# Optimization experiments

Measured on AMD Instinct MI355X. Metric: run time of the kernel, lower is better.

Reference implementation:

```python
import jax, jax.numpy as jnp
import numpy as np

N_NODES = 50000
N_EDGES = 800000
IN_CH = 256
OUT_CH = 128
HID = 2 * OUT_CH  # 256
N_GRAPHS = 64


def setup_inputs() -> dict:
    key = jax.random.key(0)
    k = jax.random.split(key, 8)
    x = jax.random.normal(k[0], (N_NODES, IN_CH), dtype=jnp.float32)
    edge_index = jax.random.randint(k[1], (2, N_EDGES), 0, N_NODES, dtype=jnp.int64)
    batch = jnp.sort(jax.random.randint(k[2], (N_NODES,), 0, N_GRAPHS, dtype=jnp.int64))
    # GCNConv parameters (glorot-ish init)
    W1 = jax.random.normal(k[3], (IN_CH, HID), dtype=jnp.float32) / np.sqrt(IN_CH)
    b1 = jnp.zeros((HID,), dtype=jnp.float32)
    W2 = jax.random.normal(k[4], (HID, OUT_CH), dtype=jnp.float32) / np.sqrt(HID)
    b2 = jnp.zeros((OUT_CH,), dtype=jnp.float32)
    return {"x": x, "W1": W1, "b1": b1, "W2": W2, "b2": b2,
            "edge_index": edge_index, "batch": batch}


def _gcn_conv(x, W, b, src, dst, n):
    """PyG GCNConv: transform, then sym-normalized aggregation with self-loops."""
    h = x @ W  # [N, F_out]
    # degree over destination nodes, including the added self-loop
    deg = jnp.zeros((n,), dtype=h.dtype).at[dst].add(1.0) + 1.0
    dinv = jax.lax.rsqrt(deg)
    norm = dinv[src] * dinv[dst]            # [E]
    agg = jnp.zeros_like(h).at[dst].add(h[src] * norm[:, None])
    agg = agg + h * (1.0 / deg)[:, None]    # self-loop contribution: deg_i^{-1}
    return agg + b


def reference(x, W1, b1, W2, b2, edge_index, batch):
    src, dst = edge_index[0], edge_index[1]
    # dropout is identity in eval mode (training=False)
    h = jax.nn.elu(_gcn_conv(x, W1, b1, src, dst, N_NODES))
    h = _gcn_conv(h, W2, b2, src, dst, N_NODES)
    # global mean pool over graphs
    ones = jnp.ones((N_NODES,), dtype=h.dtype)
    counts = jax.ops.segment_sum(ones, batch, num_segments=N_GRAPHS)
    sums = jax.ops.segment_sum(h, batch, num_segments=N_GRAPHS)
    return sums / jnp.maximum(counts, 1.0)[:, None]
```

## Files before the change

### kernel.cpp

```cpp
#include <hip/hip_runtime.h>
#include <hip/hip_bf16.h>

#define N_NODES 50000
#define N_EDGES 800000
#define IN_CH 256
#define HID 256
#define OUT_CH 128
#define N_GRAPHS 64
#define SCAN_BLOCKS 196
#define M_PAD 50048
#define POOL_CHUNK 32
#define POOL_BLOCKS ((N_NODES + POOL_CHUNK - 1) / POOL_CHUNK)
#define COUNT_BLOCKS 3125
#define CVTX_BLOCKS  12512
#define GEMM1_BLOCKS 782

typedef __bf16 bf16x8 __attribute__((ext_vector_type(8)));
typedef float f32x4 __attribute__((ext_vector_type(4)));

__device__ __forceinline__ float bf2f(unsigned short u) {
    union { unsigned int i; float f; } x; x.i = ((unsigned int)u) << 16; return x.f;
}
__device__ __forceinline__ unsigned short f2bf(float f) {
    union { float f; unsigned int i; } x; x.f = f;
    unsigned int r = x.i + 0x7FFFu + ((x.i >> 16) & 1u);
    return (unsigned short)(r >> 16);
}

__device__ __forceinline__ void load16(const void* g, void* l) {
    __builtin_amdgcn_global_load_lds(
        (const __attribute__((address_space(1))) void*)g,
        (__attribute__((address_space(3))) void*)l, 16, 0, 0);
}

__device__ __forceinline__ int rp(const int* __restrict__ rl,
                                  const int* __restrict__ boff, int i) {
    return rl[i] + boff[i >> 8];
}

__global__ __launch_bounds__(256) void count_cvtx_kernel(const int* __restrict__ ei,
                                                         int* __restrict__ cnt,
                                                         const float* __restrict__ x,
                                                         unsigned short* __restrict__ xb) {
    int b = blockIdx.x;
    if (b < COUNT_BLOCKS) {
        int e = b * 256 + threadIdx.x;
        atomicAdd(&cnt[ei[N_EDGES + e]], 1);
        return;
    }
    int i = (b - COUNT_BLOCKS) * 256 + threadIdx.x;
    ushort4 o;
    if (i < N_NODES * (IN_CH / 4)) {
        float4 v = ((const float4*)x)[i];
        o.x = f2bf(v.x); o.y = f2bf(v.y); o.z = f2bf(v.z); o.w = f2bf(v.w);
    } else {
        o = make_ushort4(0, 0, 0, 0);
    }
    ((ushort4*)xb)[i] = o;
}

__global__ __launch_bounds__(256) void scan_a_kernel(const int* __restrict__ cnt,
                                                     int* __restrict__ rl,
                                                     int* __restrict__ blocksum,
                                                     float* __restrict__ dinv,
                                                     float* __restrict__ invdeg,
                                                     int* __restrict__ fillp) {
    __shared__ int tmp[256];
    int t = threadIdx.x;
    int i = blockIdx.x * 256 + t;
    int v = (i < N_NODES) ? cnt[i] : 0;
    int x = v;
    tmp[t] = x;
    __syncthreads();
#pragma unroll
    for (int off = 1; off < 256; off <<= 1) {
        int y = (t >= off) ? tmp[t - off] : 0;
        __syncthreads();
        x += y;
        tmp[t] = x;
        __syncthreads();
    }
    if (i <= N_NODES) rl[i] = x - v;
    if (i < N_NODES) {
        float d = (float)v + 1.0f;
        dinv[i] = rsqrtf(d);
        invdeg[i] = 1.0f / d;
        fillp[i] = 0;
    }
    if (t == 255) blocksum[blockIdx.x] = x;
}

__global__ __launch_bounds__(256) void scanb_cvtw_kernel(
        const int* __restrict__ blocksum, int* __restrict__ blockoff,
        const float* __restrict__ W1, const float* __restrict__ W2,
        unsigned short* __restrict__ w1t, unsigned short* __restrict__ w2t,
        float* __restrict__ zbase ) {
    int t = threadIdx.x;
    if (blockIdx.x < 384) {
        int i = blockIdx.x * 256 + t;
        if (i < HID * IN_CH) {
            int n = i >> 8, k = i & 255;
            w1t[i] = f2bf(W1[k * HID + n]);
        } else {
            int j = i - HID * IN_CH;
            int n = j >> 8, k = j & 255;
            w2t[j] = f2bf(W2[k * OUT_CH + n]);
        }
        return;
    }
    for (int i = t; i < N_GRAPHS + N_GRAPHS * OUT_CH; i += 256)
        zbase[i] = 0.f;
    __shared__ int tmp[256];
    int v = (t < SCAN_BLOCKS) ? blocksum[t] : 0;
    int x = v;
    tmp[t] = x;
    __syncthreads();
#pragma unroll
    for (int off = 1; off < 256; off <<= 1) {
        int y = (t >= off) ? tmp[t - off] : 0;
        __syncthreads();
        x += y;
        tmp[t] = x;
        __syncthreads();
    }
    if (t < SCAN_BLOCKS) blockoff[t] = x - v;
}

__device__ __forceinline__ void gemm_body(const unsigned short* __restrict__ A,
                                          const unsigned short* __restrict__ Bt,
                                          unsigned short* __restrict__ C,
                                          int N, int bxx, int byy, char* As, char* Bs) {
    const int K = 256;
    int tid = threadIdx.x;
    int bm = bxx * 128;
    int bn = byy * 128;
    int lane = tid & 63, wave = tid >> 6;
    int lane15 = lane & 15, quad = lane >> 4;
    int wm0 = (wave >> 1) << 6;
    int wn0 = (wave & 1) << 6;

    int s1 = tid, s2 = tid + 256;
    int r1 = s1 >> 2, q1 = (s1 & 3) ^ ((r1 >> 1) & 3);
    int r2 = s2 >> 2, q2 = (s2 & 3) ^ ((r2 >> 1) & 3);
    const char* gA1 = (const char*)(A + (size_t)(bm + r1) * K) + (q1 << 4);
    const char* gA2 = (const char*)(A + (size_t)(bm + r2) * K) + (q2 << 4);
    const char* gB1 = (const char*)(Bt + (size_t)(bn + r1) * K) + (q1 << 4);
    const char* gB2 = (const char*)(Bt + (size_t)(bn + r2) * K) + (q2 << 4);
    char* lA1 = As + (wave << 10);
    char* lA2 = As + 4096 + (wave << 10);
    char* lB1 = Bs + (wave << 10);
    char* lB2 = Bs + 4096 + (wave << 10);

    int swm = (lane15 >> 1) & 3;
    f32x4 acc[4][4];
#pragma unroll
    for (int mt = 0; mt < 4; mt++)
#pragma unroll
        for (int nt = 0; nt < 4; nt++)
            acc[mt][nt] = (f32x4){0.f, 0.f, 0.f, 0.f};

    for (int k0 = 0; k0 < K; k0 += 32) {
        __syncthreads();
        load16(gA1 + (k0 << 1), lA1);
        load16(gA2 + (k0 << 1), lA2);
        load16(gB1 + (k0 << 1), lB1);
        load16(gB2 + (k0 << 1), lB2);
        __syncthreads();
        bf16x8 af[4], bfr[4];
#pragma unroll
        for (int t = 0; t < 4; t++) {
            int ra = wm0 + t * 16 + lane15;
            af[t] = *(const bf16x8*)(As + ra * 64 + ((quad ^ swm) << 4));
            int rb = wn0 + t * 16 + lane15;
            bfr[t] = *(const bf16x8*)(Bs + rb * 64 + ((quad ^ swm) << 4));
        }
#pragma unroll
        for (int mt = 0; mt < 4; mt++)
#pragma unroll
            for (int nt = 0; nt < 4; nt++)
                acc[mt][nt] = __builtin_amdgcn_mfma_f32_16x16x32_bf16(
                    af[mt], bfr[nt], acc[mt][nt], 0, 0, 0);
    }

#pragma unroll
    for (int mt = 0; mt < 4; mt++) {
        int rowb = bm + wm0 + mt * 16 + quad * 4;
#pragma unroll
        for (int nt = 0; nt < 4; nt++) {
            int col = bn + wn0 + nt * 16 + lane15;
            f32x4 a = acc[mt][nt];
            C[(size_t)(rowb + 0) * N + col] = f2bf(a[0]);
            C[(size_t)(rowb + 1) * N + col] = f2bf(a[1]);
            C[(size_t)(rowb + 2) * N + col] = f2bf(a[2]);
            C[(size_t)(rowb + 3) * N + col] = f2bf(a[3]);
        }
    }
}

__global__ __launch_bounds__(256) void fill_gemm1_kernel(
        const int* __restrict__ ei,
        const int* __restrict__ rl,
        const int* __restrict__ boff,
        int* __restrict__ fillp,
        int2* __restrict__ edge2,
        const float* __restrict__ dinv,
        const unsigned short* __restrict__ xb,
        const unsigned short* __restrict__ w1t,
        unsigned short* __restrict__ h1b) {
    __shared__ char As[8192];
    __shared__ char Bs[8192];
    int b = blockIdx.x;
    if (b < GEMM1_BLOCKS) {
        gemm_body(xb, w1t, h1b, HID, b % 391, b / 391, As, Bs);
        return;
    }
    int e = (b - GEMM1_BLOCKS) * 256 + threadIdx.x;
    if (e >= N_EDGES) return;
    int s = ei[e];
    int d = ei[N_EDGES + e];
    int p = rp(rl, boff, d) + atomicAdd(&fillp[d], 1);
    float w = dinv[s] * dinv[d];
    edge2[p] = make_int2(s, __float_as_int(w));
}

__global__ __launch_bounds__(256) void gemm_mfma_kernel(
        const unsigned short* __restrict__ A,
        const unsigned short* __restrict__ Bt,
        unsigned short* __restrict__ C,
        int N) {
    __shared__ char As[8192];
    __shared__ char Bs[8192];
    gemm_body(A, Bt, C, N, blockIdx.x, blockIdx.y, As, Bs);
}

#define ACC4(V, W) \
    acc.x += bf2f(V.x) * W; acc.y += bf2f(V.y) * W; \
    acc.z += bf2f(V.z) * W; acc.w += bf2f(V.w) * W;

__global__ __launch_bounds__(256) void agg1_kernel(const unsigned short* __restrict__ h,
                                                   const float* __restrict__ bias,
                                                   const int* __restrict__ rl,
                                                   const int* __restrict__ boff,
                                                   const int2* __restrict__ edge2,
                                                   const float* __restrict__ invdeg,
                                                   unsigned short* __restrict__ out) {
    int node = blockIdx.x * 4 + (threadIdx.x >> 6);
    if (node >= N_NODES) return;
    int lane = threadIdx.x & 63;
    const ushort4* h4 = (const ushort4*)h;
    float id = invdeg[node];
    ushort4 sv = h4[(size_t)node * 64 + lane];
    float4 acc = make_float4(bf2f(sv.x) * id, bf2f(sv.y) * id,
                             bf2f(sv.z) * id, bf2f(sv.w) * id);
    int e0 = rp(rl, boff, node);
    int e1 = rp(rl, boff, node + 1);
    int e = e0;
    for (; e + 7 < e1; e += 8) {
        int2 ed[8];
        ushort4 v[8];
#pragma unroll
        for (int j = 0; j < 8; j++) ed[j] = edge2[e + j];
#pragma unroll
        for (int j = 0; j < 8; j++) v[j] = h4[(size_t)ed[j].x * 64 + lane];
#pragma unroll
        for (int j = 0; j < 8; j++) {
            float w = __int_as_float(ed[j].y);
            ACC4(v[j], w);
        }
    }
    for (; e + 3 < e1; e += 4) {
        int2 ed[4];
        ushort4 v[4];
#pragma unroll
        for (int j = 0; j < 4; j++) ed[j] = edge2[e + j];
#pragma unroll
        for (int j = 0; j < 4; j++) v[j] = h4[(size_t)ed[j].x * 64 + lane];
#pragma unroll
        for (int j = 0; j < 4; j++) {
            float w = __int_as_float(ed[j].y);
            ACC4(v[j], w);
        }
    }
    for (; e < e1; e++) {
        int2 ed0 = edge2[e];
        float w0 = __int_as_float(ed0.y);
        ushort4 v0 = h4[(size_t)ed0.x * 64 + lane];
        ACC4(v0, w0);
    }
    float4 bb = ((const float4*)bias)[lane];
    acc.x += bb.x; acc.y += bb.y; acc.z += bb.z; acc.w += bb.w;
    acc.x = acc.x > 0.f ? acc.x : expm1f(acc.x);
    acc.y = acc.y > 0.f ? acc.y : expm1f(acc.y);
    acc.z = acc.z > 0.f ? acc.z : expm1f(acc.z);
    acc.w = acc.w > 0.f ? acc.w : expm1f(acc.w);
    ushort4 o;
    o.x = f2bf(acc.x); o.y = f2bf(acc.y); o.z = f2bf(acc.z); o.w = f2bf(acc.w);
    ((ushort4*)out)[(size_t)node * 64 + lane] = o;
}

#define ACC2(V, W) \
    acc.x += bf2f(V.x) * W; acc.y += bf2f(V.y) * W;

__global__ __launch_bounds__(256) void agg2_kernel(const unsigned short* __restrict__ h,
                                                   const float* __restrict__ bias,
                                                   const int* __restrict__ rl,
                                                   const int* __restrict__ boff,
                                                   const int2* __restrict__ edge2,
                                                   const float* __restrict__ invdeg,
                                                   unsigned short* __restrict__ out) {
    int node = blockIdx.x * 4 + (threadIdx.x >> 6);
    if (node >= N_NODES) return;
    int lane = threadIdx.x & 63;
    const ushort2* h2 = (const ushort2*)h;
    float id = invdeg[node];
    ushort2 sv = h2[(size_t)node * 64 + lane];
    float2 acc = make_float2(bf2f(sv.x) * id, bf2f(sv.y) * id);
    int e0 = rp(rl, boff, node);
    int e1 = rp(rl, boff, node + 1);
    int e = e0;
    for (; e + 7 < e1; e += 8) {
        int2 ed[8];
        ushort2 v[8];
#pragma unroll
        for (int j = 0; j < 8; j++) ed[j] = edge2[e + j];
#pragma unroll
        for (int j = 0; j < 8; j++) v[j] = h2[(size_t)ed[j].x * 64 + lane];
#pragma unroll
        for (int j = 0; j < 8; j++) {
            float w = __int_as_float(ed[j].y);
            ACC2(v[j], w);
        }
    }
    for (; e + 3 < e1; e += 4) {
        int2 ed[4];
        ushort2 v[4];
#pragma unroll
        for (int j = 0; j < 4; j++) ed[j] = edge2[e + j];
#pragma unroll
        for (int j = 0; j < 4; j++) v[j] = h2[(size_t)ed[j].x * 64 + lane];
#pragma unroll
        for (int j = 0; j < 4; j++) {
            float w = __int_as_float(ed[j].y);
            ACC2(v[j], w);
        }
    }
    for (; e < e1; e++) {
        int2 ed0 = edge2[e];
        float w0 = __int_as_float(ed0.y);
        ushort2 v0 = h2[(size_t)ed0.x * 64 + lane];
        ACC2(v0, w0);
    }
    float2 bb = ((const float2*)bias)[lane];
    acc.x += bb.x; acc.y += bb.y;
    ushort2 o;
    o.x = f2bf(acc.x); o.y = f2bf(acc.y);
    ((ushort2*)out)[(size_t)node * 64 + lane] = o;
}

__global__ __launch_bounds__(128) void pool_kernel(const unsigned short* __restrict__ h,
                                                   const int* __restrict__ batch,
                                                   float* __restrict__ pool,
                                                   float* __restrict__ gcnt) {
    int c = threadIdx.x;
    int n0 = blockIdx.x * POOL_CHUNK;
    int n1 = n0 + POOL_CHUNK;
    if (n1 > N_NODES) n1 = N_NODES;
    if (n0 >= N_NODES) return;
    float run = 0.f, cnt = 0.f;
    int g = batch[n0];
    for (int n = n0; n < n1; n++) {
        int gn = batch[n];
        if (gn != g) {
            atomicAdd(&pool[g * OUT_CH + c], run);
            if (c == 0) atomicAdd(&gcnt[g], cnt);
            run = 0.f; cnt = 0.f; g = gn;
        }
        run += bf2f(h[(size_t)n * OUT_CH + c]);
        if (c == 0) cnt += 1.f;
    }
    atomicAdd(&pool[g * OUT_CH + c], run);
    if (c == 0) atomicAdd(&gcnt[g], cnt);
}

__global__ __launch_bounds__(256) void final_kernel(const float* __restrict__ pool,
                                                    const float* __restrict__ gcnt,
                                                    float* __restrict__ out) {
    int i = blockIdx.x * 256 + threadIdx.x;
    if (i < N_GRAPHS * OUT_CH)
        out[i] = pool[i] / fmaxf(gcnt[i >> 7], 1.0f);
}

extern "C" void kernel_launch(void* const* d_in, const int* in_sizes, int n_in,
                              void* d_out, int out_size, void* d_ws, size_t ws_size,
                              hipStream_t stream) {
    const float* x  = (const float*)d_in[0];
    const float* W1 = (const float*)d_in[1];
    const float* b1 = (const float*)d_in[2];
    const float* W2 = (const float*)d_in[3];
    const float* b2 = (const float*)d_in[4];
    const int*   ei = (const int*)d_in[5];
    const int*   batch = (const int*)d_in[6];
    float* out = (float*)d_out;

    unsigned short* xb  = (unsigned short*)d_ws;
    unsigned short* h1b = xb  + (size_t)M_PAD * IN_CH;
    unsigned short* hBb = h1b + (size_t)M_PAD * HID;
    unsigned short* h2b = hBb + (size_t)M_PAD * HID;
    unsigned short* w1t = h2b + (size_t)M_PAD * OUT_CH;
    unsigned short* w2t = w1t + HID * IN_CH;
    unsigned short* hcb = xb;
    float* dinv   = (float*)(w2t + OUT_CH * HID);
    float* invdeg = dinv + N_NODES;
    int*   rl     = (int*)(invdeg + N_NODES);
    int2*  edge2  = (int2*)(rl + 50016);
    int*   cnt    = (int*)(edge2 + N_EDGES);
    int*   fillp  = cnt + N_NODES;
    float* gcnt   = (float*)(fillp + N_NODES);
    float* pool   = gcnt + N_GRAPHS;
    int*   blocksum = (int*)(pool + N_GRAPHS * OUT_CH);
    int*   blockoff = blocksum + 256;

    hipMemsetAsync(cnt, 0, (size_t)N_NODES * 4, stream);

    count_cvtx_kernel<<<COUNT_BLOCKS + CVTX_BLOCKS, 256, 0, stream>>>(ei, cnt, x, xb);
    scan_a_kernel<<<SCAN_BLOCKS, 256, 0, stream>>>(cnt, rl, blocksum, dinv, invdeg, fillp);
    scanb_cvtw_kernel<<<385, 256, 0, stream>>>(blocksum, blockoff, W1, W2, w1t, w2t, gcnt);
    fill_gemm1_kernel<<<GEMM1_BLOCKS + COUNT_BLOCKS, 256, 0, stream>>>(
        ei, rl, blockoff, fillp, edge2, dinv, xb, w1t, h1b);
    agg1_kernel<<<(N_NODES + 3) / 4, 256, 0, stream>>>(h1b, b1, rl, blockoff,
                                                       edge2, invdeg, hBb);
    dim3 g2(M_PAD / 128, OUT_CH / 128);
    gemm_mfma_kernel<<<g2, 256, 0, stream>>>(hBb, w2t, h2b, OUT_CH);
    agg2_kernel<<<(N_NODES + 3) / 4, 256, 0, stream>>>(h2b, b2, rl, blockoff,
                                                       edge2, invdeg, hcb);
    pool_kernel<<<POOL_BLOCKS, 128, 0, stream>>>(hcb, batch, pool, gcnt);
    final_kernel<<<(N_GRAPHS * OUT_CH + 255) / 256, 256, 0, stream>>>(pool, gcnt, out);
}
```

Baseline: 309.7 us.

## Fold second aggregation and mean-pool into a dense pooling-matrix GEMM

Uses linearity: the mean pool of the second GCN aggregation equals P·A_norm·H2, so a 64×N pooling-weighted adjacency matrix S is built with atomics during edge fill. S is then multiplied by a transposed H2 using MFMA with split bf16 hi/lo precision, and the partial sums are reduced. This removes the agg2 gather, the pool and the final kernels, at the cost of zeroing and streaming a 64×50048 fp32 matrix and adding 800k extra float atomics. H2 is written transposed, and agg1 now zeroes the padding rows.

Result: slower. 339.1 us (+9.5%).

```diff
diff --git a/kernel.cpp b/kernel.cpp
--- a/kernel.cpp
+++ b/kernel.cpp
@@ -9,14 +9,19 @@
 #define N_GRAPHS 64
 #define SCAN_BLOCKS 196
 #define M_PAD 50048
-#define POOL_CHUNK 32
-#define POOL_BLOCKS ((N_NODES + POOL_CHUNK - 1) / POOL_CHUNK)
 #define COUNT_BLOCKS 3125
 #define CVTX_BLOCKS  12512
+#define SZERO_BLOCKS 3128
 #define GEMM1_BLOCKS 782
+#define SELF_BLOCKS  196
+#define SROW 50048
+#define T2_BLOCKS 391
+#define T2_KC 128
+#define RED_BLOCKS 128
 
 typedef __bf16 bf16x8 __attribute__((ext_vector_type(8)));
 typedef float f32x4 __attribute__((ext_vector_type(4)));
+typedef unsigned short u16x8 __attribute__((ext_vector_type(8)));
 
 __device__ __forceinline__ float bf2f(unsigned short u) {
     union { unsigned int i; float f; } x; x.i = ((unsigned int)u) << 16; return x.f;
@@ -41,22 +46,29 @@
 __global__ __launch_bounds__(256) void count_cvtx_kernel(const int* __restrict__ ei,
                                                          int* __restrict__ cnt,
                                                          const float* __restrict__ x,
-                                                         unsigned short* __restrict__ xb) {
+                                                         unsigned short* __restrict__ xb,
+                                                         float* __restrict__ Sp) {
     int b = blockIdx.x;
     if (b < COUNT_BLOCKS) {
         int e = b * 256 + threadIdx.x;
         atomicAdd(&cnt[ei[N_EDGES + e]], 1);
         return;
     }
-    int i = (b - COUNT_BLOCKS) * 256 + threadIdx.x;
-    ushort4 o;
-    if (i < N_NODES * (IN_CH / 4)) {
-        float4 v = ((const float4*)x)[i];
-        o.x = f2bf(v.x); o.y = f2bf(v.y); o.z = f2bf(v.z); o.w = f2bf(v.w);
-    } else {
-        o = make_ushort4(0, 0, 0, 0);
-    }
-    ((ushort4*)xb)[i] = o;
+    b -= COUNT_BLOCKS;
+    if (b < CVTX_BLOCKS) {
+        int i = b * 256 + threadIdx.x;
+        ushort4 o;
+        if (i < N_NODES * (IN_CH / 4)) {
+            float4 v = ((const float4*)x)[i];
+            o.x = f2bf(v.x); o.y = f2bf(v.y); o.z = f2bf(v.z); o.w = f2bf(v.w);
+        } else {
+            o = make_ushort4(0, 0, 0, 0);
+        }
+        ((ushort4*)xb)[i] = o;
+        return;
+    }
+    int i = (b - CVTX_BLOCKS) * 256 + threadIdx.x;
+    ((f32x4*)Sp)[i] = (f32x4){0.f, 0.f, 0.f, 0.f};
 }
 
 __global__ __launch_bounds__(256) void scan_a_kernel(const int* __restrict__ cnt,
@@ -64,14 +76,19 @@
                                                      int* __restrict__ blocksum,
                                                      float* __restrict__ dinv,
                                                      float* __restrict__ invdeg,
-                                                     int* __restrict__ fillp) {
+                                                     int* __restrict__ fillp,
+                                                     const int* __restrict__ batch,
+                                                     int* __restrict__ cgr) {
     __shared__ int tmp[256];
+    __shared__ int hist[64];
     int t = threadIdx.x;
     int i = blockIdx.x * 256 + t;
+    if (t < 64) hist[t] = 0;
     int v = (i < N_NODES) ? cnt[i] : 0;
     int x = v;
     tmp[t] = x;
     __syncthreads();
+    if (i < N_NODES) atomicAdd(&hist[batch[i] & 63], 1);
 #pragma unroll
     for (int off = 1; off < 256; off <<= 1) {
         int y = (t >= off) ? tmp[t - off] : 0;
@@ -88,13 +105,14 @@
         fillp[i] = 0;
     }
     if (t == 255) blocksum[blockIdx.x] = x;
+    if (t < 64 && hist[t]) atomicAdd(&cgr[t], hist[t]);
 }
 
 __global__ __launch_bounds__(256) void scanb_cvtw_kernel(
         const int* __restrict__ blocksum, int* __restrict__ blockoff,
         const float* __restrict__ W1, const float* __restrict__ W2,
         unsigned short* __restrict__ w1t, unsigned short* __restrict__ w2t,
-        float* __restrict__ zbase ) {
+        const int* __restrict__ cgr, float* __restrict__ invc) {
     int t = threadIdx.x;
     if (blockIdx.x < 384) {
         int i = blockIdx.x * 256 + t;
@@ -108,8 +126,7 @@
         }
         return;
     }
-    for (int i = t; i < N_GRAPHS + N_GRAPHS * OUT_CH; i += 256)
-        zbase[i] = 0.f;
+    if (t < N_GRAPHS) invc[t] = 1.0f / fmaxf((float)cgr[t], 1.0f);
     __shared__ int tmp[256];
     int v = (t < SCAN_BLOCKS) ? blocksum[t] : 0;
     int x = v;
@@ -126,6 +143,7 @@
     if (t < SCAN_BLOCKS) blockoff[t] = x - v;
 }
 
+template <int TR>
 __device__ __forceinline__ void gemm_body(const unsigned short* __restrict__ A,
                                           const unsigned short* __restrict__ Bt,
                                           unsigned short* __restrict__ C,
@@ -189,10 +207,17 @@
         for (int nt = 0; nt < 4; nt++) {
             int col = bn + wn0 + nt * 16 + lane15;
             f32x4 a = acc[mt][nt];
-            C[(size_t)(rowb + 0) * N + col] = f2bf(a[0]);
-            C[(size_t)(rowb + 1) * N + col] = f2bf(a[1]);
-            C[(size_t)(rowb + 2) * N + col] = f2bf(a[2]);
-            C[(size_t)(rowb + 3) * N + col] = f2bf(a[3]);
+            if (TR == 0) {
+                C[(size_t)(rowb + 0) * N + col] = f2bf(a[0]);
+                C[(size_t)(rowb + 1) * N + col] = f2bf(a[1]);
+                C[(size_t)(rowb + 2) * N + col] = f2bf(a[2]);
+                C[(size_t)(rowb + 3) * N + col] = f2bf(a[3]);
+            } else {
+                ushort4 o;
+                o.x = f2bf(a[0]); o.y = f2bf(a[1]);
+                o.z = f2bf(a[2]); o.w = f2bf(a[3]);
+                *(ushort4*)(C + (size_t)col * M_PAD + rowb) = o;
+            }
         }
     }
 }
@@ -204,6 +229,10 @@
         int* __restrict__ fillp,
         int2* __restrict__ edge2,
         const float* __restrict__ dinv,
+        const float* __restrict__ invdeg,
+        const int* __restrict__ batch,
+        const float* __restrict__ invc,
+        float* __restrict__ Sp,
         const unsigned short* __restrict__ xb,
         const unsigned short* __restrict__ w1t,
         unsigned short* __restrict__ h1b) {
@@ -211,16 +240,26 @@
     __shared__ char Bs[8192];
     int b = blockIdx.x;
     if (b < GEMM1_BLOCKS) {
-        gemm_body(xb, w1t, h1b, HID, b % 391, b / 391, As, Bs);
-        return;
-    }
-    int e = (b - GEMM1_BLOCKS) * 256 + threadIdx.x;
-    if (e >= N_EDGES) return;
-    int s = ei[e];
-    int d = ei[N_EDGES + e];
-    int p = rp(rl, boff, d) + atomicAdd(&fillp[d], 1);
-    float w = dinv[s] * dinv[d];
-    edge2[p] = make_int2(s, __float_as_int(w));
+        gemm_body<0>(xb, w1t, h1b, HID, b % 391, b / 391, As, Bs);
+        return;
+    }
+    b -= GEMM1_BLOCKS;
+    if (b < COUNT_BLOCKS) {
+        int e = b * 256 + threadIdx.x;
+        int s = ei[e];
+        int d = ei[N_EDGES + e];
+        int p = rp(rl, boff, d) + atomicAdd(&fillp[d], 1);
+        float w = dinv[s] * dinv[d];
+        edge2[p] = make_int2(s, __float_as_int(w));
+        int gd = batch[d];
+        atomicAdd(&Sp[(size_t)gd * SROW + s], w * invc[gd]);
+        return;
+    }
+    int i = (b - COUNT_BLOCKS) * 256 + threadIdx.x;
+    if (i < N_NODES) {
+        int g = batch[i];
+        atomicAdd(&Sp[(size_t)g * SROW + i], invdeg[i] * invc[g]);
+    }
 }
 
 __global__ __launch_bounds__(256) void gemm_mfma_kernel(
@@ -230,7 +269,7 @@
         int N) {
     __shared__ char As[8192];
     __shared__ char Bs[8192];
-    gemm_body(A, Bt, C, N, blockIdx.x, blockIdx.y, As, Bs);
+    gemm_body<1>(A, Bt, C, N, blockIdx.x, blockIdx.y, As, Bs);
 }
 
 #define ACC4(V, W) \
@@ -245,8 +284,12 @@
                                                    const float* __restrict__ invdeg,
                                                    unsigned short* __restrict__ out) {
     int node = blockIdx.x * 4 + (threadIdx.x >> 6);
-    if (node >= N_NODES) return;
     int lane = threadIdx.x & 63;
+    if (node >= N_NODES) {
+        if (node < M_PAD)
+            ((ushort4*)out)[(size_t)node * 64 + lane] = make_ushort4(0, 0, 0, 0);
+        return;
+    }
     const ushort4* h4 = (const ushort4*)h;
     float id = invdeg[node];
     ushort4 sv = h4[(size_t)node * 64 + lane];
@@ -298,96 +341,84 @@
     ((ushort4*)out)[(size_t)node * 64 + lane] = o;
 }
 
-#define ACC2(V, W) \
-    acc.x += bf2f(V.x) * W; acc.y += bf2f(V.y) * W;
-
-__global__ __launch_bounds__(256) void agg2_kernel(const unsigned short* __restrict__ h,
-                                                   const float* __restrict__ bias,
-                                                   const int* __restrict__ rl,
-                                                   const int* __restrict__ boff,
-                                                   const int2* __restrict__ edge2,
-                                                   const float* __restrict__ invdeg,
-                                                   unsigned short* __restrict__ out) {
-    int node = blockIdx.x * 4 + (threadIdx.x >> 6);
-    if (node >= N_NODES) return;
-    int lane = threadIdx.x & 63;
-    const ushort2* h2 = (const ushort2*)h;
-    float id = invdeg[node];
-    ushort2 sv = h2[(size_t)node * 64 + lane];
-    float2 acc = make_float2(bf2f(sv.x) * id, bf2f(sv.y) * id);
-    int e0 = rp(rl, boff, node);
-    int e1 = rp(rl, boff, node + 1);
-    int e = e0;
-    for (; e + 7 < e1; e += 8) {
-        int2 ed[8];
-        ushort2 v[8];
-#pragma unroll
-        for (int j = 0; j < 8; j++) ed[j] = edge2[e + j];
-#pragma unroll
-        for (int j = 0; j < 8; j++) v[j] = h2[(size_t)ed[j].x * 64 + lane];
-#pragma unroll
-        for (int j = 0; j < 8; j++) {
-            float w = __int_as_float(ed[j].y);
-            ACC2(v[j], w);
-        }
-    }
-    for (; e + 3 < e1; e += 4) {
-        int2 ed[4];
-        ushort2 v[4];
-#pragma unroll
-        for (int j = 0; j < 4; j++) ed[j] = edge2[e + j];
-#pragma unroll
-        for (int j = 0; j < 4; j++) v[j] = h2[(size_t)ed[j].x * 64 + lane];
-#pragma unroll
-        for (int j = 0; j < 4; j++) {
-            float w = __int_as_float(ed[j].y);
-            ACC2(v[j], w);
-        }
-    }
-    for (; e < e1; e++) {
-        int2 ed0 = edge2[e];
-        float w0 = __int_as_float(ed0.y);
-        ushort2 v0 = h2[(size_t)ed0.x * 64 + lane];
-        ACC2(v0, w0);
-    }
-    float2 bb = ((const float2*)bias)[lane];
-    acc.x += bb.x; acc.y += bb.y;
-    ushort2 o;
-    o.x = f2bf(acc.x); o.y = f2bf(acc.y);
-    ((ushort2*)out)[(size_t)node * 64 + lane] = o;
-}
-
-__global__ __launch_bounds__(128) void pool_kernel(const unsigned short* __restrict__ h,
-                                                   const int* __restrict__ batch,
-                                                   float* __restrict__ pool,
-                                                   float* __restrict__ gcnt) {
-    int c = threadIdx.x;
-    int n0 = blockIdx.x * POOL_CHUNK;
-    int n1 = n0 + POOL_CHUNK;
-    if (n1 > N_NODES) n1 = N_NODES;
-    if (n0 >= N_NODES) return;
-    float run = 0.f, cnt = 0.f;
-    int g = batch[n0];
-    for (int n = n0; n < n1; n++) {
-        int gn = batch[n];
-        if (gn != g) {
-            atomicAdd(&pool[g * OUT_CH + c], run);
-            if (c == 0) atomicAdd(&gcnt[g], cnt);
-            run = 0.f; cnt = 0.f; g = gn;
-        }
-        run += bf2f(h[(size_t)n * OUT_CH + c]);
-        if (c == 0) cnt += 1.f;
-    }
-    atomicAdd(&pool[g * OUT_CH + c], run);
-    if (c == 0) atomicAdd(&gcnt[g], cnt);
-}
-
-__global__ __launch_bounds__(256) void final_kernel(const float* __restrict__ pool,
-                                                    const float* __restrict__ gcnt,
+__global__ __launch_bounds__(256) void t2_kernel(const float* __restrict__ Sp,
+                                                 const unsigned short* __restrict__ h2t,
+                                                 float* __restrict__ part) {
+    int b = blockIdx.x;
+    int k0 = b * T2_KC;
+    int tid = threadIdx.x;
+    int lane = tid & 63, wave = tid >> 6;
+    int lane15 = lane & 15, quad = lane >> 4;
+    int cb = wave << 5;
+    f32x4 acc[4][2];
+#pragma unroll
+    for (int m = 0; m < 4; m++) {
+        acc[m][0] = (f32x4){0.f, 0.f, 0.f, 0.f};
+        acc[m][1] = (f32x4){0.f, 0.f, 0.f, 0.f};
+    }
+    const unsigned short* hr0 = h2t + (size_t)(cb + lane15) * M_PAD;
+    const unsigned short* hr1 = h2t + (size_t)(cb + 16 + lane15) * M_PAD;
+#pragma unroll
+    for (int ks = 0; ks < T2_KC / 32; ks++) {
+        int k = k0 + ks * 32 + quad * 8;
+        bf16x8 b0 = *(const bf16x8*)(hr0 + k);
+        bf16x8 b1 = *(const bf16x8*)(hr1 + k);
+#pragma unroll
+        for (int m = 0; m < 4; m++) {
+            const float* ap = Sp + (size_t)(m * 16 + lane15) * SROW + k;
+            f32x4 v0 = *(const f32x4*)ap;
+            f32x4 v1 = *(const f32x4*)(ap + 4);
+            u16x8 hu, lu;
+#pragma unroll
+            for (int j = 0; j < 4; j++) {
+                unsigned int e0 = __float_as_uint(v0[j]);
+                hu[j] = (unsigned short)(e0 >> 16);
+                lu[j] = f2bf(v0[j] - __uint_as_float(e0 & 0xFFFF0000u));
+                unsigned int e1 = __float_as_uint(v1[j]);
+                hu[j + 4] = (unsigned short)(e1 >> 16);
+                lu[j + 4] = f2bf(v1[j] - __uint_as_float(e1 & 0xFFFF0000u));
+            }
+            bf16x8 ah = __builtin_bit_cast(bf16x8, hu);
+            bf16x8 al = __builtin_bit_cast(bf16x8, lu);
+            acc[m][0] = __builtin_amdgcn_mfma_f32_16x16x32_bf16(ah, b0, acc[m][0], 0, 0, 0);
+            acc[m][0] = __builtin_amdgcn_mfma_f32_16x16x32_bf16(al, b0, acc[m][0], 0, 0, 0);
+            acc[m][1] = __builtin_amdgcn_mfma_f32_16x16x32_bf16(ah, b1, acc[m][1], 0, 0, 0);
+            acc[m][1] = __builtin_amdgcn_mfma_f32_16x16x32_bf16(al, b1, acc[m][1], 0, 0, 0);
+        }
+    }
+    float* pb = part + (size_t)b * (N_GRAPHS * OUT_CH);
+#pragma unroll
+    for (int m = 0; m < 4; m++) {
+        int g0 = m * 16 + quad * 4;
+#pragma unroll
+        for (int nt = 0; nt < 2; nt++) {
+            int c = cb + nt * 16 + lane15;
+            f32x4 a = acc[m][nt];
+#pragma unroll
+            for (int j = 0; j < 4; j++)
+                pb[(g0 + j) * OUT_CH + c] = a[j];
+        }
+    }
+}
+
+__global__ __launch_bounds__(256) void t2red_kernel(const float* __restrict__ part,
+                                                    const float* __restrict__ b2,
+                                                    const int* __restrict__ cgr,
                                                     float* __restrict__ out) {
-    int i = blockIdx.x * 256 + threadIdx.x;
-    if (i < N_GRAPHS * OUT_CH)
-        out[i] = pool[i] / fmaxf(gcnt[i >> 7], 1.0f);
+    __shared__ float red[4][64];
+    int tid = threadIdx.x;
+    int q = tid >> 6, l = tid & 63;
+    int o = blockIdx.x * 64 + l;
+    float s = 0.f;
+    for (int i = q; i < T2_BLOCKS; i += 4)
+        s += part[(size_t)i * (N_GRAPHS * OUT_CH) + o];
+    red[q][l] = s;
+    __syncthreads();
+    if (tid < 64) {
+        float tot = red[0][l] + red[1][l] + red[2][l] + red[3][l];
+        int g = o >> 7, c = o & 127;
+        out[o] = (cgr[g] > 0) ? tot + b2[c] : 0.f;
+    }
 }
 
 extern "C" void kernel_launch(void* const* d_in, const int* in_sizes, int n_in,
@@ -405,34 +436,36 @@
     unsigned short* xb  = (unsigned short*)d_ws;
     unsigned short* h1b = xb  + (size_t)M_PAD * IN_CH;
     unsigned short* hBb = h1b + (size_t)M_PAD * HID;
-    unsigned short* h2b = hBb + (size_t)M_PAD * HID;
-    unsigned short* w1t = h2b + (size_t)M_PAD * OUT_CH;
+    unsigned short* h2t = hBb + (size_t)M_PAD * HID;
+    unsigned short* w1t = h2t + (size_t)OUT_CH * M_PAD;
     unsigned short* w2t = w1t + HID * IN_CH;
-    unsigned short* hcb = xb;
     float* dinv   = (float*)(w2t + OUT_CH * HID);
     float* invdeg = dinv + N_NODES;
     int*   rl     = (int*)(invdeg + N_NODES);
     int2*  edge2  = (int2*)(rl + 50016);
     int*   cnt    = (int*)(edge2 + N_EDGES);
-    int*   fillp  = cnt + N_NODES;
-    float* gcnt   = (float*)(fillp + N_NODES);
-    float* pool   = gcnt + N_GRAPHS;
-    int*   blocksum = (int*)(pool + N_GRAPHS * OUT_CH);
+    int*   cgr    = cnt + N_NODES;
+    int*   fillp  = cgr + N_GRAPHS;
+    float* Sp     = (float*)(fillp + N_NODES);
+    int*   blocksum = (int*)(Sp + (size_t)N_GRAPHS * SROW);
     int*   blockoff = blocksum + 256;
-
-    hipMemsetAsync(cnt, 0, (size_t)N_NODES * 4, stream);
-
-    count_cvtx_kernel<<<COUNT_BLOCKS + CVTX_BLOCKS, 256, 0, stream>>>(ei, cnt, x, xb);
-    scan_a_kernel<<<SCAN_BLOCKS, 256, 0, stream>>>(cnt, rl, blocksum, dinv, invdeg, fillp);
-    scanb_cvtw_kernel<<<385, 256, 0, stream>>>(blocksum, blockoff, W1, W2, w1t, w2t, gcnt);
-    fill_gemm1_kernel<<<GEMM1_BLOCKS + COUNT_BLOCKS, 256, 0, stream>>>(
-        ei, rl, blockoff, fillp, edge2, dinv, xb, w1t, h1b);
-    agg1_kernel<<<(N_NODES + 3) / 4, 256, 0, stream>>>(h1b, b1, rl, blockoff,
-                                                       edge2, invdeg, hBb);
+    float* invc   = (float*)(blockoff + 256);
+    float* part   = (float*)h1b;
+
+    hipMemsetAsync(cnt, 0, (size_t)(N_NODES + N_GRAPHS) * 4, stream);
+
+    count_cvtx_kernel<<<COUNT_BLOCKS + CVTX_BLOCKS + SZERO_BLOCKS, 256, 0, stream>>>(
+        ei, cnt, x, xb, Sp);
+    scan_a_kernel<<<SCAN_BLOCKS, 256, 0, stream>>>(cnt, rl, blocksum, dinv, invdeg,
+                                                   fillp, batch, cgr);
+    scanb_cvtw_kernel<<<385, 256, 0, stream>>>(blocksum, blockoff, W1, W2, w1t, w2t,
+                                               cgr, invc);
+    fill_gemm1_kernel<<<GEMM1_BLOCKS + COUNT_BLOCKS + SELF_BLOCKS, 256, 0, stream>>>(
+        ei, rl, blockoff, fillp, edge2, dinv, invdeg, batch, invc, Sp, xb, w1t, h1b);
+    agg1_kernel<<<M_PAD / 4, 256, 0, stream>>>(h1b, b1, rl, blockoff,
+                                               edge2, invdeg, hBb);
     dim3 g2(M_PAD / 128, OUT_CH / 128);
-    gemm_mfma_kernel<<<g2, 256, 0, stream>>>(hBb, w2t, h2b, OUT_CH);
-    agg2_kernel<<<(N_NODES + 3) / 4, 256, 0, stream>>>(h2b, b2, rl, blockoff,
-                                                       edge2, invdeg, hcb);
-    pool_kernel<<<POOL_BLOCKS, 128, 0, stream>>>(hcb, batch, pool, gcnt);
-    final_kernel<<<(N_GRAPHS * OUT_CH + 255) / 256, 256, 0, stream>>>(pool, gcnt, out);
-}
+    gemm_mfma_kernel<<<g2, 256, 0, stream>>>(hBb, w2t, h2t, OUT_CH);
+    t2_kernel<<<T2_BLOCKS, 256, 0, stream>>>(Sp, h2t, part);
+    t2red_kernel<<<RED_BLOCKS, 256, 0, stream>>>(part, b2, cgr, out);
+}
```

## Pool per graph via segment offsets, unroll aggregation by 16, vectorize bf16 unpack

Applied to the files above, without the earlier changes.

Segment start offsets for each graph are computed from the sorted batch array inside the scan kernel. Pooling then runs as one block per graph with a shared-memory reduction that writes the mean directly, which removes the atomic pool kernel, the final divide kernel and the zero-init of the pool buffers. Both aggregation kernels gain a 16-edge unrolled gather loop to keep more loads in flight, and unpack bf16 pairs with shift/mask on 32-bit words into vector FMAs. The price is higher register pressure in the aggregation kernels, and pooling now runs on only 64 blocks.

Measured after the change: 321.8 us. 3.9% more time.

```diff
diff --git a/kernel.cpp b/kernel.cpp
--- a/kernel.cpp
+++ b/kernel.cpp
@@ -9,14 +9,13 @@
 #define N_GRAPHS 64
 #define SCAN_BLOCKS 196
 #define M_PAD 50048
-#define POOL_CHUNK 32
-#define POOL_BLOCKS ((N_NODES + POOL_CHUNK - 1) / POOL_CHUNK)
 #define COUNT_BLOCKS 3125
 #define CVTX_BLOCKS  12512
 #define GEMM1_BLOCKS 782
 
 typedef __bf16 bf16x8 __attribute__((ext_vector_type(8)));
 typedef float f32x4 __attribute__((ext_vector_type(4)));
+typedef float f32x2 __attribute__((ext_vector_type(2)));
 
 __device__ __forceinline__ float bf2f(unsigned short u) {
     union { unsigned int i; float f; } x; x.i = ((unsigned int)u) << 16; return x.f;
@@ -25,6 +24,13 @@
     union { float f; unsigned int i; } x; x.f = f;
     unsigned int r = x.i + 0x7FFFu + ((x.i >> 16) & 1u);
     return (unsigned short)(r >> 16);
+}
+
+__device__ __forceinline__ float lo_f(unsigned int u) {
+    return __uint_as_float(u << 16);
+}
+__device__ __forceinline__ float hi_f(unsigned int u) {
+    return __uint_as_float(u & 0xFFFF0000u);
 }
 
 __device__ __forceinline__ void load16(const void* g, void* l) {
@@ -64,7 +70,9 @@
                                                      int* __restrict__ blocksum,
                                                      float* __restrict__ dinv,
                                                      float* __restrict__ invdeg,
-                                                     int* __restrict__ fillp) {
+                                                     int* __restrict__ fillp,
+                                                     const int* __restrict__ batch,
+                                                     int* __restrict__ rstart) {
     __shared__ int tmp[256];
     int t = threadIdx.x;
     int i = blockIdx.x * 256 + t;
@@ -72,6 +80,13 @@
     int x = v;
     tmp[t] = x;
     __syncthreads();
+    if (i < N_NODES) {
+        int bg = batch[i];
+        int bp = (i > 0) ? batch[i - 1] : -1;
+        for (int g = bp + 1; g <= bg; g++) rstart[g] = i;
+        if (i == N_NODES - 1)
+            for (int g = bg + 1; g <= N_GRAPHS; g++) rstart[g] = N_NODES;
+    }
 #pragma unroll
     for (int off = 1; off < 256; off <<= 1) {
         int y = (t >= off) ? tmp[t - off] : 0;
@@ -93,8 +108,7 @@
 __global__ __launch_bounds__(256) void scanb_cvtw_kernel(
         const int* __restrict__ blocksum, int* __restrict__ blockoff,
         const float* __restrict__ W1, const float* __restrict__ W2,
-        unsigned short* __restrict__ w1t, unsigned short* __restrict__ w2t,
-        float* __restrict__ zbase ) {
+        unsigned short* __restrict__ w1t, unsigned short* __restrict__ w2t) {
     int t = threadIdx.x;
     if (blockIdx.x < 384) {
         int i = blockIdx.x * 256 + t;
@@ -108,8 +122,6 @@
         }
         return;
     }
-    for (int i = t; i < N_GRAPHS + N_GRAPHS * OUT_CH; i += 256)
-        zbase[i] = 0.f;
     __shared__ int tmp[256];
     int v = (t < SCAN_BLOCKS) ? blocksum[t] : 0;
     int x = v;
@@ -233,10 +245,6 @@
     gemm_body(A, Bt, C, N, blockIdx.x, blockIdx.y, As, Bs);
 }
 
-#define ACC4(V, W) \
-    acc.x += bf2f(V.x) * W; acc.y += bf2f(V.y) * W; \
-    acc.z += bf2f(V.z) * W; acc.w += bf2f(V.w) * W;
-
 __global__ __launch_bounds__(256) void agg1_kernel(const unsigned short* __restrict__ h,
                                                    const float* __restrict__ bias,
                                                    const int* __restrict__ rl,
@@ -247,17 +255,32 @@
     int node = blockIdx.x * 4 + (threadIdx.x >> 6);
     if (node >= N_NODES) return;
     int lane = threadIdx.x & 63;
-    const ushort4* h4 = (const ushort4*)h;
+    const uint2* h4 = (const uint2*)h;
     float id = invdeg[node];
-    ushort4 sv = h4[(size_t)node * 64 + lane];
-    float4 acc = make_float4(bf2f(sv.x) * id, bf2f(sv.y) * id,
-                             bf2f(sv.z) * id, bf2f(sv.w) * id);
+    uint2 sv = h4[(size_t)node * 64 + lane];
+    f32x4 acc = (f32x4){lo_f(sv.x) * id, hi_f(sv.x) * id,
+                        lo_f(sv.y) * id, hi_f(sv.y) * id};
     int e0 = rp(rl, boff, node);
     int e1 = rp(rl, boff, node + 1);
     int e = e0;
+    for (; e + 15 < e1; e += 16) {
+        int2 ed[16];
+        uint2 v[16];
+#pragma unroll
+        for (int j = 0; j < 16; j++) ed[j] = edge2[e + j];
+#pragma unroll
+        for (int j = 0; j < 16; j++) v[j] = h4[(size_t)ed[j].x * 64 + lane];
+#pragma unroll
+        for (int j = 0; j < 16; j++) {
+            float w = __int_as_float(ed[j].y);
+            f32x4 vf = (f32x4){lo_f(v[j].x), hi_f(v[j].x),
+                               lo_f(v[j].y), hi_f(v[j].y)};
+            acc += vf * w;
+        }
+    }
     for (; e + 7 < e1; e += 8) {
         int2 ed[8];
-        ushort4 v[8];
+        uint2 v[8];
 #pragma unroll
         for (int j = 0; j < 8; j++) ed[j] = edge2[e + j];
 #pragma unroll
@@ -265,12 +288,14 @@
 #pragma unroll
         for (int j = 0; j < 8; j++) {
             float w = __int_as_float(ed[j].y);
-            ACC4(v[j], w);
+            f32x4 vf = (f32x4){lo_f(v[j].x), hi_f(v[j].x),
+                               lo_f(v[j].y), hi_f(v[j].y)};
+            acc += vf * w;
         }
     }
     for (; e + 3 < e1; e += 4) {
         int2 ed[4];
-        ushort4 v[4];
+        uint2 v[4];
 #pragma unroll
         for (int j = 0; j < 4; j++) ed[j] = edge2[e + j];
 #pragma unroll
@@ -278,28 +303,28 @@
 #pragma unroll
         for (int j = 0; j < 4; j++) {
             float w = __int_as_float(ed[j].y);
-            ACC4(v[j], w);
+            f32x4 vf = (f32x4){lo_f(v[j].x), hi_f(v[j].x),
+                               lo_f(v[j].y), hi_f(v[j].y)};
+            acc += vf * w;
         }
     }
     for (; e < e1; e++) {
         int2 ed0 = edge2[e];
         float w0 = __int_as_float(ed0.y);
-        ushort4 v0 = h4[(size_t)ed0.x * 64 + lane];
-        ACC4(v0, w0);
+        uint2 v0 = h4[(size_t)ed0.x * 64 + lane];
+        f32x4 vf = (f32x4){lo_f(v0.x), hi_f(v0.x), lo_f(v0.y), hi_f(v0.y)};
+        acc += vf * w0;
     }
     float4 bb = ((const float4*)bias)[lane];
-    acc.x += bb.x; acc.y += bb.y; acc.z += bb.z; acc.w += bb.w;
-    acc.x = acc.x > 0.f ? acc.x : expm1f(acc.x);
-    acc.y = acc.y > 0.f ? acc.y : expm1f(acc.y);
-    acc.z = acc.z > 0.f ? acc.z : expm1f(acc.z);
-    acc.w = acc.w > 0.f ? acc.w : expm1f(acc.w);
+    acc[0] += bb.x; acc[1] += bb.y; acc[2] += bb.z; acc[3] += bb.w;
+    acc[0] = acc[0] > 0.f ? acc[0] : expm1f(acc[0]);
+    acc[1] = acc[1] > 0.f ? acc[1] : expm1f(acc[1]);
+    acc[2] = acc[2] > 0.f ? acc[2] : expm1f(acc[2]);
+    acc[3] = acc[3] > 0.f ? acc[3] : expm1f(acc[3]);
     ushort4 o;
-    o.x = f2bf(acc.x); o.y = f2bf(acc.y); o.z = f2bf(acc.z); o.w = f2bf(acc.w);
+    o.x = f2bf(acc[0]); o.y = f2bf(acc[1]); o.z = f2bf(acc[2]); o.w = f2bf(acc[3]);
     ((ushort4*)out)[(size_t)node * 64 + lane] = o;
 }
-
-#define ACC2(V, W) \
-    acc.x += bf2f(V.x) * W; acc.y += bf2f(V.y) * W;
 
 __global__ __launch_bounds__(256) void agg2_kernel(const unsigned short* __restrict__ h,
                                                    const float* __restrict__ bias,
@@ -311,16 +336,29 @@
     int node = blockIdx.x * 4 + (threadIdx.x >> 6);
     if (node >= N_NODES) return;
     int lane = threadIdx.x & 63;
-    const ushort2* h2 = (const ushort2*)h;
+    const unsigned int* h2 = (const unsigned int*)h;
     float id = invdeg[node];
-    ushort2 sv = h2[(size_t)node * 64 + lane];
-    float2 acc = make_float2(bf2f(sv.x) * id, bf2f(sv.y) * id);
+    unsigned int sv = h2[(size_t)node * 64 + lane];
+    f32x2 acc = (f32x2){lo_f(sv) * id, hi_f(sv) * id};
     int e0 = rp(rl, boff, node);
     int e1 = rp(rl, boff, node + 1);
     int e = e0;
+    for (; e + 15 < e1; e += 16) {
+        int2 ed[16];
+        unsigned int v[16];
+#pragma unroll
+        for (int j = 0; j < 16; j++) ed[j] = edge2[e + j];
+#pragma unroll
+        for (int j = 0; j < 16; j++) v[j] = h2[(size_t)ed[j].x * 64 + lane];
+#pragma unroll
+        for (int j = 0; j < 16; j++) {
+            float w = __int_as_float(ed[j].y);
+            acc += (f32x2){lo_f(v[j]), hi_f(v[j])} * w;
+        }
+    }
     for (; e + 7 < e1; e += 8) {
         int2 ed[8];
-        ushort2 v[8];
+        unsigned int v[8];
 #pragma unroll
         for (int j = 0; j < 8; j++) ed[j] = edge2[e + j];
 #pragma unroll
@@ -328,12 +366,12 @@
 #pragma unroll
         for (int j = 0; j < 8; j++) {
             float w = __int_as_float(ed[j].y);
-            ACC2(v[j], w);
+            acc += (f32x2){lo_f(v[j]), hi_f(v[j])} * w;
         }
     }
     for (; e + 3 < e1; e += 4) {
         int2 ed[4];
-        ushort2 v[4];
+        unsigned int v[4];
 #pragma unroll
         for (int j = 0; j < 4; j++) ed[j] = edge2[e + j];
 #pragma unroll
@@ -341,53 +379,48 @@
 #pragma unroll
         for (int j = 0; j < 4; j++) {
             float w = __int_as_float(ed[j].y);
-            ACC2(v[j], w);
+            acc += (f32x2){lo_f(v[j]), hi_f(v[j])} * w;
         }
     }
     for (; e < e1; e++) {
         int2 ed0 = edge2[e];
         float w0 = __int_as_float(ed0.y);
-        ushort2 v0 = h2[(size_t)ed0.x * 64 + lane];
-        ACC2(v0, w0);
+        unsigned int v0 = h2[(size_t)ed0.x * 64 + lane];
+        acc += (f32x2){lo_f(v0), hi_f(v0)} * w0;
     }
     float2 bb = ((const float2*)bias)[lane];
-    acc.x += bb.x; acc.y += bb.y;
+    acc[0] += bb.x; acc[1] += bb.y;
     ushort2 o;
-    o.x = f2bf(acc.x); o.y = f2bf(acc.y);
+    o.x = f2bf(acc[0]); o.y = f2bf(acc[1]);
     ((ushort2*)out)[(size_t)node * 64 + lane] = o;
 }
 
-__global__ __launch_bounds__(128) void pool_kernel(const unsigned short* __restrict__ h,
-                                                   const int* __restrict__ batch,
-                                                   float* __restrict__ pool,
-                                                   float* __restrict__ gcnt) {
-    int c = threadIdx.x;
-    int n0 = blockIdx.x * POOL_CHUNK;
-    int n1 = n0 + POOL_CHUNK;
-    if (n1 > N_NODES) n1 = N_NODES;
-    if (n0 >= N_NODES) return;
-    float run = 0.f, cnt = 0.f;
-    int g = batch[n0];
-    for (int n = n0; n < n1; n++) {
-        int gn = batch[n];
-        if (gn != g) {
-            atomicAdd(&pool[g * OUT_CH + c], run);
-            if (c == 0) atomicAdd(&gcnt[g], cnt);
-            run = 0.f; cnt = 0.f; g = gn;
-        }
-        run += bf2f(h[(size_t)n * OUT_CH + c]);
-        if (c == 0) cnt += 1.f;
-    }
-    atomicAdd(&pool[g * OUT_CH + c], run);
-    if (c == 0) atomicAdd(&gcnt[g], cnt);
-}
-
-__global__ __launch_bounds__(256) void final_kernel(const float* __restrict__ pool,
-                                                    const float* __restrict__ gcnt,
-                                                    float* __restrict__ out) {
-    int i = blockIdx.x * 256 + threadIdx.x;
-    if (i < N_GRAPHS * OUT_CH)
-        out[i] = pool[i] / fmaxf(gcnt[i >> 7], 1.0f);
+__global__ __launch_bounds__(512) void pool_kernel(const unsigned short* __restrict__ h,
+                                                   const int* __restrict__ rstart,
+                                                   float* __restrict__ out) {
+    int g = blockIdx.x;
+    int n0 = rstart[g], n1 = rstart[g + 1];
+    int c2 = threadIdx.x & 63;
+    int row = threadIdx.x >> 6;
+    const unsigned int* h2 = (const unsigned int*)h;
+    float ax = 0.f, ay = 0.f;
+    for (int n = n0 + row; n < n1; n += 8) {
+        unsigned int u = h2[(size_t)n * 64 + c2];
+        ax += lo_f(u);
+        ay += hi_f(u);
+    }
+    __shared__ float red[8][128];
+    red[row][c2 * 2] = ax;
+    red[row][c2 * 2 + 1] = ay;
+    __syncthreads();
+    if (threadIdx.x < 128) {
+        int c = threadIdx.x;
+        float s = 0.f;
+#pragma unroll
+        for (int r = 0; r < 8; r++) s += red[r][c];
+        int cn = n1 - n0;
+        out[g * OUT_CH + c] = (cn > 0) ? s / (float)cn : 0.f;
+    }
 }
 
 extern "C" void kernel_launch(void* const* d_in, const int* in_sizes, int n_in,
@@ -415,16 +448,16 @@
     int2*  edge2  = (int2*)(rl + 50016);
     int*   cnt    = (int*)(edge2 + N_EDGES);
     int*   fillp  = cnt + N_NODES;
-    float* gcnt   = (float*)(fillp + N_NODES);
-    float* pool   = gcnt + N_GRAPHS;
-    int*   blocksum = (int*)(pool + N_GRAPHS * OUT_CH);
+    int*   blocksum = fillp + N_NODES;
     int*   blockoff = blocksum + 256;
+    int*   rstart   = blockoff + 256;
 
     hipMemsetAsync(cnt, 0, (size_t)N_NODES * 4, stream);
 
     count_cvtx_kernel<<<COUNT_BLOCKS + CVTX_BLOCKS, 256, 0, stream>>>(ei, cnt, x, xb);
-    scan_a_kernel<<<SCAN_BLOCKS, 256, 0, stream>>>(cnt, rl, blocksum, dinv, invdeg, fillp);
-    scanb_cvtw_kernel<<<385, 256, 0, stream>>>(blocksum, blockoff, W1, W2, w1t, w2t, gcnt);
+    scan_a_kernel<<<SCAN_BLOCKS, 256, 0, stream>>>(cnt, rl, blocksum, dinv, invdeg,
+                                                   fillp, batch, rstart);
+    scanb_cvtw_kernel<<<385, 256, 0, stream>>>(blocksum, blockoff, W1, W2, w1t, w2t);
     fill_gemm1_kernel<<<GEMM1_BLOCKS + COUNT_BLOCKS, 256, 0, stream>>>(
         ei, rl, blockoff, fillp, edge2, dinv, xb, w1t, h1b);
     agg1_kernel<<<(N_NODES + 3) / 4, 256, 0, stream>>>(h1b, b1, rl, blockoff,
@@ -433,6 +466,5 @@
     gemm_mfma_kernel<<<g2, 256, 0, stream>>>(hBb, w2t, h2b, OUT_CH);
     agg2_kernel<<<(N_NODES + 3) / 4, 256, 0, stream>>>(h2b, b2, rl, blockoff,
                                                        edge2, invdeg, hcb);
-    pool_kernel<<<POOL_BLOCKS, 128, 0, stream>>>(hcb, batch, pool, gcnt);
-    final_kernel<<<(N_GRAPHS * OUT_CH + 255) / 256, 256, 0, stream>>>(pool, gcnt, out);
-}
+    pool_kernel<<<N_GRAPHS, 512, 0, stream>>>(hcb, rstart, out);
+}
```
